# Kernel tuning notes

Measured on AMD Instinct MI355X. Metric: run time of the kernel, lower is better.

The kernel has to match this reference:

```python
import jax, jax.numpy as jnp
import numpy as np

HIDDEN = 1024
NUM_HEADS = 16
HEAD_DIM = HIDDEN // NUM_HEADS  # 64
MLP_HIDDEN = 4096
RMS_EPS = 1e-6


def setup_inputs() -> dict:
    key = jax.random.key(0)
    ks = jax.random.split(key, 4)
    B, L = 2, 2048
    x = jax.random.normal(ks[0], (B, L, HIDDEN), dtype=jnp.float32)
    pe = jax.random.normal(ks[1], (1, 1, L, HEAD_DIM // 2, 2, 2), dtype=jnp.float32)
    W1 = jax.random.normal(ks[2], (HIDDEN, 3 * HIDDEN + MLP_HIDDEN), dtype=jnp.float32) * (HIDDEN ** -0.5)
    b1 = jnp.zeros((3 * HIDDEN + MLP_HIDDEN,), dtype=jnp.float32)
    W2 = jax.random.normal(ks[3], (HIDDEN + MLP_HIDDEN, HIDDEN), dtype=jnp.float32) * ((HIDDEN + MLP_HIDDEN) ** -0.5)
    b2 = jnp.zeros((HIDDEN,), dtype=jnp.float32)
    q_scale = jnp.ones((HEAD_DIM,), dtype=jnp.float32)
    k_scale = jnp.ones((HEAD_DIM,), dtype=jnp.float32)
    return {"x": x, "pe": pe, "W1": W1, "b1": b1, "W2": W2, "b2": b2,
            "q_scale": q_scale, "k_scale": k_scale}


def _rms_norm(t, scale):
    # RMSNorm over last dim (head_dim) with learnable scale (flux QKNorm)
    rrms = jax.lax.rsqrt(jnp.mean(jnp.square(t), axis=-1, keepdims=True) + RMS_EPS)
    return t * rrms * scale


def _apply_rope(xq, xk, pe):
    # pe: [1,1,L,D/2,2,2]; x*: [B,H,L,D]
    def rope(t):
        t_ = t.reshape(*t.shape[:-1], -1, 1, 2)  # [B,H,L,D/2,1,2]
        out = pe[..., 0] * t_[..., 0] + pe[..., 1] * t_[..., 1]  # [B,H,L,D/2,2]
        return out.reshape(*t.shape)
    return rope(xq), rope(xk)


def reference(x, pe, W1, b1, W2, b2, q_scale, k_scale):
    B, L, _ = x.shape
    h = x @ W1 + b1  # [B,L,3H+Mh]
    qkv, mlp = h[..., : 3 * HIDDEN], h[..., 3 * HIDDEN:]
    # 'B L (K H D) -> K B H L D'
    qkv = qkv.reshape(B, L, 3, NUM_HEADS, HEAD_DIM).transpose(2, 0, 3, 1, 4)
    q, k, v = qkv[0], qkv[1], qkv[2]
    q = _rms_norm(q, q_scale)
    k = _rms_norm(k, k_scale)
    q, k = _apply_rope(q, k, pe)
    scale = HEAD_DIM ** -0.5
    scores = jnp.einsum('bhqd,bhkd->bhqk', q, k) * scale
    attn = jnp.einsum('bhqk,bhkd->bhqd', jax.nn.softmax(scores, axis=-1), v)
    attn = attn.transpose(0, 2, 1, 3).reshape(B, L, HIDDEN)  # 'B H L D -> B L (H D)'
    out = jnp.concatenate((attn, jax.nn.gelu(mlp)), axis=2) @ W2 + b2
    return out
```

## Files before the change

### kernel.cpp

```cpp
#include <hip/hip_runtime.h>

typedef __bf16 bf16;
typedef __bf16 bf16x8 __attribute__((ext_vector_type(8)));
typedef float f32x4 __attribute__((ext_vector_type(4)));
typedef float f32x16 __attribute__((ext_vector_type(16)));

#define GLDS16(gp, lp) __builtin_amdgcn_global_load_lds( \
    (__attribute__((address_space(1))) void*)(gp), \
    (__attribute__((address_space(3))) void*)(lp), 16, 0, 0)

__device__ inline float ex2(float x) { return exp2f(x); }

__device__ inline float gelu_fast(float x) {
    float t = ex2(-2.3022081702f * (x + 0.044715f * x * x * x));
    return x * __builtin_amdgcn_rcpf(1.0f + t);
}


__global__ void f2b_kernel(const float* __restrict__ src, bf16* __restrict__ dst, long n) {
    long i = ((long)blockIdx.x * 256 + threadIdx.x) * 4;
    if (i + 3 < n) {
        float4 v = *(const float4*)&src[i];
        dst[i + 0] = (bf16)v.x;
        dst[i + 1] = (bf16)v.y;
        dst[i + 2] = (bf16)v.z;
        dst[i + 3] = (bf16)v.w;
    }
}

__global__ __launch_bounds__(256) void transpose_f2b(const float* __restrict__ W,
                                                     bf16* __restrict__ WT,
                                                     int K, int N) {
    __shared__ float tile[32][33];
    int tx = threadIdx.x & 31;
    int ty = threadIdx.x >> 5;
    int n0 = blockIdx.x * 32;
    int k0 = blockIdx.y * 32;
#pragma unroll
    for (int i = 0; i < 4; ++i)
        tile[ty + i * 8][tx] = W[(long)(k0 + ty + i * 8) * N + n0 + tx];
    __syncthreads();
#pragma unroll
    for (int i = 0; i < 4; ++i)
        WT[(long)(n0 + ty + i * 8) * K + k0 + tx] = (bf16)tile[tx][ty + i * 8];
}

#define STA(tile, ch) if ((tile) < NT) { \
    const bf16* s_ = gA + (tile) * 64 + (ch) * 32; \
    char* d_ = lds + ((tile) & 1) * 65536 + (ch) * 16384 + tid * 16; \
    GLDS16(s_, d_); GLDS16(s_ + (long)128 * K, d_ + 8192); }

#define STB(tile, ch) if ((tile) < NT) { \
    const bf16* s_ = gB + (tile) * 64 + (ch) * 32; \
    char* d_ = lds + ((tile) & 1) * 65536 + 32768 + (ch) * 16384 + tid * 16; \
    GLDS16(s_, d_); GLDS16(s_ + (long)128 * K, d_ + 8192); }

#define PH(tb, mh, kh, RB, STAGE_STMT, WAITN) do { \
    { const char* Ab_ = lds + (tb) * 65536 + (kh) * 16384; \
      const char* Bb_ = lds + (tb) * 65536 + 32768 + (kh) * 16384; \
      if (RB) { \
        _Pragma("unroll") for (int n_ = 0; n_ < 4; ++n_) \
          bfrag[n_] = *(const bf16x8*)(Bb_ + (wc * 64 + n_ * 16 + fr) * 64 + aslot); } \
      _Pragma("unroll") for (int i_ = 0; i_ < 4; ++i_) \
          afrag[i_] = *(const bf16x8*)(Ab_ + (wr * 128 + (mh) * 64 + i_ * 16 + fr) * 64 + aslot); \
    } \
    STAGE_STMT; \
    asm volatile("s_waitcnt vmcnt(" #WAITN ")" ::: "memory"); \
    asm volatile("s_barrier" ::: "memory"); \
    __builtin_amdgcn_s_setprio(1); \
    _Pragma("unroll") for (int n_ = 0; n_ < 4; ++n_) \
      _Pragma("unroll") for (int i_ = 0; i_ < 4; ++i_) \
        acc[(mh) * 4 + i_][n_] = __builtin_amdgcn_mfma_f32_16x16x32_bf16(afrag[i_], bfrag[n_], acc[(mh) * 4 + i_][n_], 0, 0, 0); \
    __builtin_amdgcn_s_setprio(0); \
    asm volatile("s_barrier" ::: "memory"); \
} while (0)

template <int EPI>
__global__ __launch_bounds__(512, 2) void gemm8p(const bf16* __restrict__ A_,
                                                 const bf16* __restrict__ BT_,
                                                 const float* __restrict__ bias,
                                                 void* __restrict__ C0,
                                                 void* __restrict__ C1,
                                                 int M, int N, int K, int kch) {
    __shared__ __align__(16) char lds[131072];

    int bx, by, k0base = 0;
    if (EPI == 0) {
        int bid = blockIdx.x;
        int swz = (bid & 7) * 56 + (bid >> 3);
        bx = swz % 16; by = swz / 16;
    } else {
        bx = blockIdx.x; by = blockIdx.y;
        k0base = blockIdx.z * kch;
    }
    int bm = bx * 256, bn = by * 256;
    int NT = kch >> 6;

    int tid = threadIdx.x;
    int w = tid >> 6, l = tid & 63;
    int wr = w >> 2, wc = w & 3;
    int fr = l & 15;
    int aslot = (((l >> 4) ^ ((fr >> 1) & 3)) << 4);

    int srow0 = tid >> 2;
    int sgoff = (((tid & 3) ^ ((srow0 >> 1) & 3)) << 3);
    const bf16* gA = A_ + (long)(bm + srow0) * K + k0base + sgoff;
    const bf16* gB = BT_ + (long)(bn + srow0) * K + k0base + sgoff;

    f32x4 acc[8][4] = {};
    bf16x8 bfrag[4];
    bf16x8 afrag[4];

    STA(0, 0); STA(0, 1); STB(0, 0); STB(0, 1);
    STB(1, 0); STA(1, 0); STB(1, 1);
    asm volatile("s_waitcnt vmcnt(0)" ::: "memory");
    asm volatile("s_barrier" ::: "memory");

    int NI = NT >> 1;
    for (int i = 0; i < NI; ++i) {
        int t1 = 2 * i + 1, t2 = 2 * i + 2, t3 = 2 * i + 3;
        if (i == NI - 1) {
            PH(0, 0, 0, true, STA(t1, 1), 0);
        } else {
            PH(0, 0, 0, true, STA(t1, 1), 10);
        }
        PH(0, 1, 0, false, STB(t2, 0), 10);
        PH(0, 0, 1, true,  STA(t2, 0), 10);
        PH(0, 1, 1, false, STB(t2, 1), 10);
        PH(1, 0, 0, true,  STA(t2, 1), 10);
        PH(1, 1, 0, false, STB(t3, 0), 10);
        PH(1, 0, 1, true,  STA(t3, 0), 10);
        PH(1, 1, 1, false, STB(t3, 1), 10);
    }

    int r4 = (l >> 4) * 4;
    if (EPI == 0) {
        bf16* hp = (bf16*)C0;
        bf16* cat = (bf16*)C1;
        bool gel = (bn >= 3072);
#pragma unroll
        for (int mi = 0; mi < 8; ++mi) {
            int row = bm + wr * 128 + mi * 16 + r4;
#pragma unroll
            for (int n = 0; n < 4; ++n) {
                int col = bn + wc * 64 + n * 16 + fr;
                float bv = bias[col];
#pragma unroll
                for (int r = 0; r < 4; ++r) {
                    float v = acc[mi][n][r] + bv;
                    if (gel) {
                        cat[(long)(row + r) * 5120 + 1024 + col - 3072] = (bf16)gelu_fast(v);
                    } else {
                        hp[(long)(row + r) * N + col] = (bf16)v;
                    }
                }
            }
        }
    } else {
        float* cz = (float*)C0 + (long)blockIdx.z * M * N;
#pragma unroll
        for (int mi = 0; mi < 8; ++mi) {
            int row = bm + wr * 128 + mi * 16 + r4;
#pragma unroll
            for (int n = 0; n < 4; ++n) {
                int col = bn + wc * 64 + n * 16 + fr;
#pragma unroll
                for (int r = 0; r < 4; ++r)
                    cz[(long)(row + r) * N + col] = acc[mi][n][r];
            }
        }
    }
}

__global__ __launch_bounds__(256) void reduce4_kernel(const float* __restrict__ part,
                                                      const float* __restrict__ b2,
                                                      float* __restrict__ out) {
    const long stride4 = 4096L * 1024 / 4;
#pragma unroll
    for (int it = 0; it < 2; ++it) {
        long i4 = (long)blockIdx.x * 512 + it * 256 + threadIdx.x;
        float4 s = *(const float4*)&b2[(i4 * 4) & 1023];
        const float4* p = (const float4*)part;
#pragma unroll
        for (int z = 0; z < 4; ++z) {
            float4 v = p[z * stride4 + i4];
            s.x += v.x; s.y += v.y; s.z += v.z; s.w += v.w;
        }
        *(float4*)&out[i4 * 4] = s;
    }
}

__global__ __launch_bounds__(256) void qkv_kernel(const bf16* __restrict__ h,
                                                  const float* __restrict__ pe,
                                                  const float* __restrict__ qsc_,
                                                  const float* __restrict__ ksc_,
                                                  bf16* __restrict__ qo,
                                                  bf16* __restrict__ ko) {
    int t = blockIdx.x;
    int b = t >> 11;
    int lpos = t & 2047;
    int wv = threadIdx.x >> 6;
    int d = threadIdx.x & 63;
    const bf16* hrow = h + (long)t * 7168;
    float pe0 = pe[lpos * 128 + (d >> 1) * 4 + (d & 1) * 2 + 0];
    float pe1 = pe[lpos * 128 + (d >> 1) * 4 + (d & 1) * 2 + 1];
    float qsc = qsc_[d], ksc = ksc_[d];
#pragma unroll 1
    for (int it = 0; it < 4; ++it) {
        int hh = wv * 4 + it;
        float qv = (float)hrow[hh * 64 + d];
        float kv = (float)hrow[1024 + hh * 64 + d];
        float ssq = qv * qv, ssk = kv * kv;
#pragma unroll
        for (int off = 1; off < 64; off <<= 1) {
            ssq += __shfl_xor(ssq, off, 64);
            ssk += __shfl_xor(ssk, off, 64);
        }
        float qn = qv * rsqrtf(ssq * (1.0f / 64.0f) + 1e-6f) * qsc;
        float kn = kv * rsqrtf(ssk * (1.0f / 64.0f) + 1e-6f) * ksc;
        float qe = __shfl(qn, d & 62, 64), qodd = __shfl(qn, d | 1, 64);
        float ke = __shfl(kn, d & 62, 64), kodd = __shfl(kn, d | 1, 64);
        float qr = (pe0 * qe + pe1 * qodd) * 0.18033688011112042f;
        float kr = pe0 * ke + pe1 * kodd;
        long base = ((long)(b * 16 + hh) * 2048 + lpos) * 64 + d;
        qo[base] = (bf16)qr;
        ko[base] = (bf16)kr;
    }
}

__global__ __launch_bounds__(256) void vtrans_kernel(const bf16* __restrict__ h,
                                                     bf16* __restrict__ vT) {
    __shared__ unsigned short tile[64 * 65];
    int bh = blockIdx.x;
    int b = bh >> 4, hh = bh & 15;
    int l0 = blockIdx.y * 64;
    int tid = threadIdx.x;

    int r = tid >> 3, c = tid & 7;
#pragma unroll
    for (int p = 0; p < 2; ++p) {
        int row = r + p * 32;
        const bf16* src = h + (long)(b * 2048 + l0 + row) * 7168 + 2048 + hh * 64 + c * 8;
        bf16x8 v = *(const bf16x8*)src;
        union { bf16x8 v; unsigned short s[8]; } u; u.v = v;
#pragma unroll
        for (int e = 0; e < 8; ++e) tile[row * 65 + c * 8 + e] = u.s[e];
    }
    __syncthreads();
#pragma unroll
    for (int p = 0; p < 2; ++p) {
        int idx = tid + p * 256;
        int d = idx >> 3, kg = idx & 7;
        union { bf16x8 v; unsigned short s[8]; } u;
#pragma unroll
        for (int e = 0; e < 8; ++e) u.s[e] = tile[(kg * 8 + e) * 65 + d];
        *(bf16x8*)&vT[((long)bh * 64 + d) * 2048 + l0 + kg * 8] = u.v;
    }
}

__global__ __launch_bounds__(256) void attn_kernel(const bf16* __restrict__ qg,
                                                   const bf16* __restrict__ kg_,
                                                   const bf16* __restrict__ vT,
                                                   bf16* __restrict__ cat) {
    __shared__ __align__(16) char lds[49152];
    char* Kl0 = lds;
    char* Kl1 = lds + 8192;
    char* Vl0 = lds + 16384;
    char* Vl1 = lds + 24576;

    int bidx = blockIdx.x;
    int bh = bidx & 31;
    int qblk = bidx >> 5;
    int b = bh >> 4, hh = bh & 15;
    int tid = threadIdx.x;
    int wv = tid >> 6, l = tid & 63;
    int h = l >> 5, ln = l & 31;
    int sw = (ln & 7) << 4;

    char* Pw = lds + 32768 + wv * 4096;

    const bf16* qbase = qg + ((long)bh * 2048 + qblk * 128 + wv * 32 + ln) * 64 + h * 8;
    bf16x8 qf[4];
#pragma unroll
    for (int ds = 0; ds < 4; ++ds) qf[ds] = *(const bf16x8*)(qbase + ds * 16);

    f32x16 Oa0 = {}, Oa1 = {};
    float m = -1e30f, lsum = 0.0f;

    int kr = tid >> 3, kg = tid & 7;
    int swb = (kg * 16) ^ ((kr & 7) << 4);
    const bf16* gK = kg_ + ((long)bh * 2048 + kr) * 64 + kg * 8;
    const bf16* gV = vT + ((long)bh * 64 + kr) * 2048 + kg * 8;

    bf16x8 rk0 = *(const bf16x8*)gK;
    bf16x8 rk1 = *(const bf16x8*)(gK + 32 * 64);
    bf16x8 rv0 = *(const bf16x8*)gV;
    bf16x8 rv1 = *(const bf16x8*)(gV + 32 * 2048);
    *(bf16x8*)(Kl0 + kr * 128 + swb) = rk0;
    *(bf16x8*)(Kl0 + (kr + 32) * 128 + swb) = rk1;
    *(bf16x8*)(Vl0 + kr * 128 + swb) = rv0;
    *(bf16x8*)(Vl0 + (kr + 32) * 128 + swb) = rv1;
    __syncthreads();

    int c = 0;
    for (int t = 0; t < 32; ++t) {
        if (t < 31) {
            rk0 = *(const bf16x8*)(gK + (long)(t + 1) * 4096);
            rk1 = *(const bf16x8*)(gK + (long)(t + 1) * 4096 + 32 * 64);
            rv0 = *(const bf16x8*)(gV + (t + 1) * 64);
            rv1 = *(const bf16x8*)(gV + (t + 1) * 64 + 32 * 2048);
        }
        const char* Kc = c ? Kl1 : Kl0;
        const char* Vc = c ? Vl1 : Vl0;

        f32x16 S0 = {}, S1 = {};
        __builtin_amdgcn_s_setprio(1);
#pragma unroll
        for (int ds = 0; ds < 4; ++ds) {
            bf16x8 kf0 = *(const bf16x8*)(Kc + ln * 128 + ((ds * 32 + h * 16) ^ sw));
            bf16x8 kf1 = *(const bf16x8*)(Kc + (32 + ln) * 128 + ((ds * 32 + h * 16) ^ sw));
            S0 = __builtin_amdgcn_mfma_f32_32x32x16_bf16(kf0, qf[ds], S0, 0, 0, 0);
            S1 = __builtin_amdgcn_mfma_f32_32x32x16_bf16(kf1, qf[ds], S1, 0, 0, 0);
        }
        __builtin_amdgcn_s_setprio(0);

        float tmax = S0[0];
#pragma unroll
        for (int r = 1; r < 16; ++r) tmax = fmaxf(tmax, S0[r]);
#pragma unroll
        for (int r = 0; r < 16; ++r) tmax = fmaxf(tmax, S1[r]);
        tmax = fmaxf(tmax, __shfl_xor(tmax, 32, 64));

        if (!__all(tmax - m <= 8.0f)) {
            float mn = fmaxf(m, tmax);
            float es = ex2(m - mn);
            lsum *= es;
            m = mn;
#pragma unroll
            for (int r = 0; r < 16; ++r) {
                int rowq = (r & 3) + 8 * (r >> 2) + 4 * h;
                float esr = __shfl(es, rowq, 64);
                Oa0[r] *= esr;
                Oa1[r] *= esr;
            }
        }

        float ps = 0.0f;
#pragma unroll
        for (int kvt = 0; kvt < 2; ++kvt) {
            float p[16];
#pragma unroll
            for (int r = 0; r < 16; ++r) {
                float v = ex2((kvt ? S1[r] : S0[r]) - m);
                p[r] = v;
                ps += v;
            }
#pragma unroll
            for (int i = 0; i < 8; ++i) {
                union { bf16 bb[2]; unsigned u; } pr;
                pr.bb[0] = (bf16)p[2 * i];
                pr.bb[1] = (bf16)p[2 * i + 1];
                int kv = ((2 * i) & 3) + 8 * (i >> 1) + 4 * h + 32 * kvt;
                *(unsigned*)(Pw + ln * 128 + ((kv * 2) ^ sw)) = pr.u;
            }
        }
        lsum += ps + __shfl_xor(ps, 32, 64);

        asm volatile("s_waitcnt lgkmcnt(0)" ::: "memory");

        bf16x8 pa[4];
#pragma unroll
        for (int s = 0; s < 4; ++s)
            pa[s] = *(const bf16x8*)(Pw + ln * 128 + ((s * 32 + h * 16) ^ sw));

        __builtin_amdgcn_s_setprio(1);
#pragma unroll
        for (int s = 0; s < 4; ++s) {
            bf16x8 vf0 = *(const bf16x8*)(Vc + ln * 128 + ((s * 32 + h * 16) ^ sw));
            bf16x8 vf1 = *(const bf16x8*)(Vc + (32 + ln) * 128 + ((s * 32 + h * 16) ^ sw));
            Oa0 = __builtin_amdgcn_mfma_f32_32x32x16_bf16(pa[s], vf0, Oa0, 0, 0, 0);
            Oa1 = __builtin_amdgcn_mfma_f32_32x32x16_bf16(pa[s], vf1, Oa1, 0, 0, 0);
        }
        __builtin_amdgcn_s_setprio(0);

        __syncthreads();
        if (t < 31) {
            char* Kn = c ? Kl0 : Kl1;
            char* Vn = c ? Vl0 : Vl1;
            *(bf16x8*)(Kn + kr * 128 + swb) = rk0;
            *(bf16x8*)(Kn + (kr + 32) * 128 + swb) = rk1;
            *(bf16x8*)(Vn + kr * 128 + swb) = rv0;
            *(bf16x8*)(Vn + (kr + 32) * 128 + swb) = rv1;
        }
        __syncthreads();
        c ^= 1;
    }

#pragma unroll
    for (int r = 0; r < 16; ++r) {
        int rowq = (r & 3) + 8 * (r >> 2) + 4 * h;
        float ls = __shfl(lsum, rowq, 64);
        float inv = 1.0f / ls;
        long trow = (long)b * 2048 + qblk * 128 + wv * 32 + rowq;
        cat[trow * 5120 + hh * 64 + ln] = (bf16)(Oa0[r] * inv);
        cat[trow * 5120 + hh * 64 + 32 + ln] = (bf16)(Oa1[r] * inv);
    }
}


extern "C" void kernel_launch(void* const* d_in, const int* in_sizes, int n_in,
                              void* d_out, int out_size, void* d_ws, size_t ws_size,
                              hipStream_t stream) {
    const float* x  = (const float*)d_in[0];
    const float* pe = (const float*)d_in[1];
    const float* W1 = (const float*)d_in[2];
    const float* b1 = (const float*)d_in[3];
    const float* W2 = (const float*)d_in[4];
    const float* b2 = (const float*)d_in[5];
    const float* qs = (const float*)d_in[6];
    const float* ks = (const float*)d_in[7];
    float* out = (float*)d_out;

    char* ws = (char*)d_ws;
    bf16* xb  = (bf16*)(ws);
    bf16* w1t = (bf16*)(ws + 8388608);
    bf16* w2t = (bf16*)(ws + 23068672);
    bf16* h   = (bf16*)(ws + 33554432);
    bf16* qb  = (bf16*)(ws + 92274688);
    bf16* kb  = (bf16*)(ws + 100663296);
    bf16* vT  = (bf16*)(ws + 109051904);
    bf16* cat = (bf16*)(ws + 117440512);
    float* part = (float*)(ws + 33554432);

    f2b_kernel<<<4096, 256, 0, stream>>>(x, xb, 4194304L);
    transpose_f2b<<<dim3(224, 32), 256, 0, stream>>>(W1, w1t, 1024, 7168);
    transpose_f2b<<<dim3(32, 160), 256, 0, stream>>>(W2, w2t, 5120, 1024);

    gemm8p<0><<<dim3(448), 512, 0, stream>>>(xb, w1t, b1, h, cat, 4096, 7168, 1024, 1024);

    qkv_kernel<<<4096, 256, 0, stream>>>(h, pe, qs, ks, qb, kb);
    vtrans_kernel<<<dim3(32, 32), 256, 0, stream>>>(h, vT);

    attn_kernel<<<512, 256, 0, stream>>>(qb, kb, vT, cat);

    gemm8p<1><<<dim3(16, 4, 4), 512, 0, stream>>>(cat, w2t, nullptr, part, nullptr, 4096, 1024, 5120, 1280);
    reduce4_kernel<<<2048, 256, 0, stream>>>(part, b2, out);
}
```

Baseline: 264.2 us.

## Fuse QK RMSNorm and RoPE epilogue into first GEMM with simpler tile

The first projection GEMM now applies bias, per-head RMSNorm, RoPE and the q scale in its epilogue and writes q/k directly in head-major layout. V goes to a compact buffer and the GELU branch still writes into the concat buffer. This removes the separate qkv kernel and the round trip through the wide h buffer. In exchange it replaces the heavily pipelined 256x256 double-buffered GEMM with a plain single-buffered 128x128 kernel that waits on every load and has no load/compute overlap, so the GEMM mainloop may lose efficiency.

New measurement: 253.4 us. 1.04x faster.

```diff
diff --git a/kernel.cpp b/kernel.cpp
--- a/kernel.cpp
+++ b/kernel.cpp
@@ -43,6 +43,141 @@
 #pragma unroll
     for (int i = 0; i < 4; ++i)
         WT[(long)(n0 + ty + i * 8) * K + k0 + tx] = (bf16)tile[tx][ty + i * 8];
+}
+
+__global__ __launch_bounds__(256) void gemm1_fused(const bf16* __restrict__ A,
+                                                   const bf16* __restrict__ BT,
+                                                   const float* __restrict__ bias,
+                                                   const float* __restrict__ pe,
+                                                   const float* __restrict__ qsc,
+                                                   const float* __restrict__ ksc,
+                                                   bf16* __restrict__ qb_,
+                                                   bf16* __restrict__ kb_,
+                                                   bf16* __restrict__ vsrc,
+                                                   bf16* __restrict__ cat,
+                                                   int K) {
+    __shared__ __align__(16) char Asm[128 * 128];
+    __shared__ __align__(16) char Bsm[128 * 128];
+    int tid = threadIdx.x;
+    int w = tid >> 6, l = tid & 63;
+    int wr = w >> 1, wc = w & 1;
+    int bm = blockIdx.x * 128;
+    int bn = blockIdx.y * 128;
+
+    f32x4 acc[4][4] = {};
+
+    int fr = l & 15;
+    int g16 = (l >> 4) * 16;
+    int xsw = (fr & 7) << 4;
+
+    int srow = tid >> 3;
+    int sg8 = ((tid & 7) ^ (srow & 7)) * 8;
+    int dstoff = tid * 16;
+
+    int nk = K >> 6;
+    for (int kt = 0; kt < nk; ++kt) {
+        int k0 = kt * 64;
+#pragma unroll
+        for (int gg = 0; gg < 4; ++gg) {
+            const bf16* ga = A + (long)(bm + gg * 32 + srow) * K + k0 + sg8;
+            GLDS16(ga, Asm + gg * 4096 + dstoff);
+            const bf16* gb = BT + (long)(bn + gg * 32 + srow) * K + k0 + sg8;
+            GLDS16(gb, Bsm + gg * 4096 + dstoff);
+        }
+        asm volatile("s_waitcnt vmcnt(0)" ::: "memory");
+        __syncthreads();
+
+#pragma unroll
+        for (int kk = 0; kk < 2; ++kk) {
+            int koff = (kk * 64 + g16) ^ xsw;
+            bf16x8 af[4], bfr[4];
+#pragma unroll
+            for (int m = 0; m < 4; ++m)
+                af[m] = *(const bf16x8*)(Asm + (wr * 64 + m * 16 + fr) * 128 + koff);
+#pragma unroll
+            for (int n = 0; n < 4; ++n)
+                bfr[n] = *(const bf16x8*)(Bsm + (wc * 64 + n * 16 + fr) * 128 + koff);
+#pragma unroll
+            for (int m = 0; m < 4; ++m)
+#pragma unroll
+                for (int n = 0; n < 4; ++n)
+                    acc[m][n] = __builtin_amdgcn_mfma_f32_16x16x32_bf16(af[m], bfr[n], acc[m][n], 0, 0, 0);
+        }
+        __syncthreads();
+    }
+
+    int orow0 = bm + wr * 64;
+    int ocol0 = bn + wc * 64;
+
+    if (bn < 2048) {
+        bool isq = (bn < 1024);
+        const float* sc = isq ? qsc : ksc;
+        bf16* dst = isq ? qb_ : kb_;
+#pragma unroll
+        for (int m = 0; m < 4; ++m) {
+#pragma unroll
+            for (int r = 0; r < 4; ++r) {
+                int row = orow0 + m * 16 + (l >> 4) * 4 + r;
+                int lpos = row & 2047;
+                int bb = row >> 11;
+                float v[4];
+                float ss = 0.0f;
+#pragma unroll
+                for (int n = 0; n < 4; ++n) {
+                    int col = ocol0 + n * 16 + fr;
+                    v[n] = acc[m][n][r] + bias[col];
+                    ss += v[n] * v[n];
+                }
+#pragma unroll
+                for (int off = 1; off < 16; off <<= 1)
+                    ss += __shfl_xor(ss, off, 16);
+                float rr = rsqrtf(ss * (1.0f / 64.0f) + 1e-6f);
+#pragma unroll
+                for (int n = 0; n < 4; ++n) {
+                    int col = ocol0 + n * 16 + fr;
+                    int d = col & 63;
+                    int hh = (col & 1023) >> 6;
+                    float qn = v[n] * rr * sc[d];
+                    float pv = __shfl_xor(qn, 1, 16);
+                    float qe = (d & 1) ? pv : qn;
+                    float qo = (d & 1) ? qn : pv;
+                    float pe0 = pe[lpos * 128 + (d >> 1) * 4 + (d & 1) * 2 + 0];
+                    float pe1 = pe[lpos * 128 + (d >> 1) * 4 + (d & 1) * 2 + 1];
+                    float ov = pe0 * qe + pe1 * qo;
+                    if (isq) ov *= 0.18033688011112042f;
+                    dst[((long)(bb * 16 + hh) * 2048 + lpos) * 64 + d] = (bf16)ov;
+                }
+            }
+        }
+    } else if (bn < 3072) {
+#pragma unroll
+        for (int m = 0; m < 4; ++m) {
+            int row = orow0 + m * 16 + (l >> 4) * 4;
+#pragma unroll
+            for (int n = 0; n < 4; ++n) {
+                int col = ocol0 + n * 16 + fr;
+                float bv = bias[col];
+#pragma unroll
+                for (int r = 0; r < 4; ++r)
+                    vsrc[(long)(row + r) * 1024 + col - 2048] = (bf16)(acc[m][n][r] + bv);
+            }
+        }
+    } else {
+#pragma unroll
+        for (int m = 0; m < 4; ++m) {
+            int row = orow0 + m * 16 + (l >> 4) * 4;
+#pragma unroll
+            for (int n = 0; n < 4; ++n) {
+                int col = ocol0 + n * 16 + fr;
+                float bv = bias[col];
+#pragma unroll
+                for (int r = 0; r < 4; ++r) {
+                    float v = acc[m][n][r] + bv;
+                    cat[(long)(row + r) * 5120 + 1024 + col - 3072] = (bf16)gelu_fast(v);
+                }
+            }
+        }
+    }
 }
 
 #define STA(tile, ch) if ((tile) < NT) { \
@@ -75,24 +210,14 @@
     asm volatile("s_barrier" ::: "memory"); \
 } while (0)
 
-template <int EPI>
-__global__ __launch_bounds__(512, 2) void gemm8p(const bf16* __restrict__ A_,
-                                                 const bf16* __restrict__ BT_,
-                                                 const float* __restrict__ bias,
-                                                 void* __restrict__ C0,
-                                                 void* __restrict__ C1,
-                                                 int M, int N, int K, int kch) {
+__global__ __launch_bounds__(512, 2) void gemm8p_sk(const bf16* __restrict__ A_,
+                                                    const bf16* __restrict__ BT_,
+                                                    float* __restrict__ part,
+                                                    int M, int N, int K, int kch) {
     __shared__ __align__(16) char lds[131072];
 
-    int bx, by, k0base = 0;
-    if (EPI == 0) {
-        int bid = blockIdx.x;
-        int swz = (bid & 7) * 56 + (bid >> 3);
-        bx = swz % 16; by = swz / 16;
-    } else {
-        bx = blockIdx.x; by = blockIdx.y;
-        k0base = blockIdx.z * kch;
-    }
+    int bx = blockIdx.x, by = blockIdx.y;
+    int k0base = blockIdx.z * kch;
     int bm = bx * 256, bn = by * 256;
     int NT = kch >> 6;
 
@@ -133,41 +258,17 @@
         PH(1, 1, 1, false, STB(t3, 1), 10);
     }
 
+    float* cz = part + (long)blockIdx.z * M * N;
     int r4 = (l >> 4) * 4;
-    if (EPI == 0) {
-        bf16* hp = (bf16*)C0;
-        bf16* cat = (bf16*)C1;
-        bool gel = (bn >= 3072);
-#pragma unroll
-        for (int mi = 0; mi < 8; ++mi) {
-            int row = bm + wr * 128 + mi * 16 + r4;
-#pragma unroll
-            for (int n = 0; n < 4; ++n) {
-                int col = bn + wc * 64 + n * 16 + fr;
-                float bv = bias[col];
-#pragma unroll
-                for (int r = 0; r < 4; ++r) {
-                    float v = acc[mi][n][r] + bv;
-                    if (gel) {
-                        cat[(long)(row + r) * 5120 + 1024 + col - 3072] = (bf16)gelu_fast(v);
-                    } else {
-                        hp[(long)(row + r) * N + col] = (bf16)v;
-                    }
-                }
-            }
-        }
-    } else {
-        float* cz = (float*)C0 + (long)blockIdx.z * M * N;
-#pragma unroll
-        for (int mi = 0; mi < 8; ++mi) {
-            int row = bm + wr * 128 + mi * 16 + r4;
-#pragma unroll
-            for (int n = 0; n < 4; ++n) {
-                int col = bn + wc * 64 + n * 16 + fr;
-#pragma unroll
-                for (int r = 0; r < 4; ++r)
-                    cz[(long)(row + r) * N + col] = acc[mi][n][r];
-            }
+#pragma unroll
+    for (int mi = 0; mi < 8; ++mi) {
+        int row = bm + wr * 128 + mi * 16 + r4;
+#pragma unroll
+        for (int n = 0; n < 4; ++n) {
+            int col = bn + wc * 64 + n * 16 + fr;
+#pragma unroll
+            for (int r = 0; r < 4; ++r)
+                cz[(long)(row + r) * N + col] = acc[mi][n][r];
         }
     }
 }
@@ -190,45 +291,7 @@
     }
 }
 
-__global__ __launch_bounds__(256) void qkv_kernel(const bf16* __restrict__ h,
-                                                  const float* __restrict__ pe,
-                                                  const float* __restrict__ qsc_,
-                                                  const float* __restrict__ ksc_,
-                                                  bf16* __restrict__ qo,
-                                                  bf16* __restrict__ ko) {
-    int t = blockIdx.x;
-    int b = t >> 11;
-    int lpos = t & 2047;
-    int wv = threadIdx.x >> 6;
-    int d = threadIdx.x & 63;
-    const bf16* hrow = h + (long)t * 7168;
-    float pe0 = pe[lpos * 128 + (d >> 1) * 4 + (d & 1) * 2 + 0];
-    float pe1 = pe[lpos * 128 + (d >> 1) * 4 + (d & 1) * 2 + 1];
-    float qsc = qsc_[d], ksc = ksc_[d];
-#pragma unroll 1
-    for (int it = 0; it < 4; ++it) {
-        int hh = wv * 4 + it;
-        float qv = (float)hrow[hh * 64 + d];
-        float kv = (float)hrow[1024 + hh * 64 + d];
-        float ssq = qv * qv, ssk = kv * kv;
-#pragma unroll
-        for (int off = 1; off < 64; off <<= 1) {
-            ssq += __shfl_xor(ssq, off, 64);
-            ssk += __shfl_xor(ssk, off, 64);
-        }
-        float qn = qv * rsqrtf(ssq * (1.0f / 64.0f) + 1e-6f) * qsc;
-        float kn = kv * rsqrtf(ssk * (1.0f / 64.0f) + 1e-6f) * ksc;
-        float qe = __shfl(qn, d & 62, 64), qodd = __shfl(qn, d | 1, 64);
-        float ke = __shfl(kn, d & 62, 64), kodd = __shfl(kn, d | 1, 64);
-        float qr = (pe0 * qe + pe1 * qodd) * 0.18033688011112042f;
-        float kr = pe0 * ke + pe1 * kodd;
-        long base = ((long)(b * 16 + hh) * 2048 + lpos) * 64 + d;
-        qo[base] = (bf16)qr;
-        ko[base] = (bf16)kr;
-    }
-}
-
-__global__ __launch_bounds__(256) void vtrans_kernel(const bf16* __restrict__ h,
+__global__ __launch_bounds__(256) void vtrans_kernel(const bf16* __restrict__ vsrc,
                                                      bf16* __restrict__ vT) {
     __shared__ unsigned short tile[64 * 65];
     int bh = blockIdx.x;
@@ -240,7 +303,7 @@
 #pragma unroll
     for (int p = 0; p < 2; ++p) {
         int row = r + p * 32;
-        const bf16* src = h + (long)(b * 2048 + l0 + row) * 7168 + 2048 + hh * 64 + c * 8;
+        const bf16* src = vsrc + (long)(b * 2048 + l0 + row) * 1024 + hh * 64 + c * 8;
         bf16x8 v = *(const bf16x8*)src;
         union { bf16x8 v; unsigned short s[8]; } u; u.v = v;
 #pragma unroll
@@ -422,27 +485,27 @@
     float* out = (float*)d_out;
 
     char* ws = (char*)d_ws;
-    bf16* xb  = (bf16*)(ws);
-    bf16* w1t = (bf16*)(ws + 8388608);
-    bf16* w2t = (bf16*)(ws + 23068672);
-    bf16* h   = (bf16*)(ws + 33554432);
-    bf16* qb  = (bf16*)(ws + 92274688);
-    bf16* kb  = (bf16*)(ws + 100663296);
-    bf16* vT  = (bf16*)(ws + 109051904);
-    bf16* cat = (bf16*)(ws + 117440512);
+    bf16* xb   = (bf16*)(ws);
+    bf16* w1t  = (bf16*)(ws + 8388608);
+    bf16* w2t  = (bf16*)(ws + 23068672);
+    bf16* vsrc = (bf16*)(ws + 33554432);
+    bf16* qb   = (bf16*)(ws + 92274688);
+    bf16* kb   = (bf16*)(ws + 100663296);
+    bf16* vT   = (bf16*)(ws + 109051904);
+    bf16* cat  = (bf16*)(ws + 117440512);
     float* part = (float*)(ws + 33554432);
 
     f2b_kernel<<<4096, 256, 0, stream>>>(x, xb, 4194304L);
     transpose_f2b<<<dim3(224, 32), 256, 0, stream>>>(W1, w1t, 1024, 7168);
     transpose_f2b<<<dim3(32, 160), 256, 0, stream>>>(W2, w2t, 5120, 1024);
 
-    gemm8p<0><<<dim3(448), 512, 0, stream>>>(xb, w1t, b1, h, cat, 4096, 7168, 1024, 1024);
-
-    qkv_kernel<<<4096, 256, 0, stream>>>(h, pe, qs, ks, qb, kb);
-    vtrans_kernel<<<dim3(32, 32), 256, 0, stream>>>(h, vT);
+    gemm1_fused<<<dim3(32, 56), 256, 0, stream>>>(xb, w1t, b1, pe, qs, ks,
+                                                  qb, kb, vsrc, cat, 1024);
+
+    vtrans_kernel<<<dim3(32, 32), 256, 0, stream>>>(vsrc, vT);
 
     attn_kernel<<<512, 256, 0, stream>>>(qb, kb, vT, cat);
 
-    gemm8p<1><<<dim3(16, 4, 4), 512, 0, stream>>>(cat, w2t, nullptr, part, nullptr, 4096, 1024, 5120, 1280);
+    gemm8p_sk<<<dim3(16, 4, 4), 512, 0, stream>>>(cat, w2t, part, 4096, 1024, 5120, 1280);
     reduce4_kernel<<<2048, 256, 0, stream>>>(part, b2, out);
 }
```
